# Performance work log

Measured on AMD Instinct MI355X. Metric: run time of the kernel, lower is better.

## Reference

```python
import jax, jax.numpy as jnp
import numpy as np

B, S, E, H = 2, 2048, 1024, 16
DH = E // H  # 64


def setup_inputs() -> dict:
    key = jax.random.key(0)
    ks = jax.random.split(key, 9)
    sc = 1.0 / np.sqrt(E)
    return {
        "x": jax.random.normal(ks[0], (B, S, E), dtype=jnp.float32),
        "Wq": jax.random.normal(ks[1], (E, E), dtype=jnp.float32) * sc,
        "bq": jax.random.normal(ks[2], (E,), dtype=jnp.float32) * 0.02,
        "Wk": jax.random.normal(ks[3], (E, E), dtype=jnp.float32) * sc,
        "bk": jax.random.normal(ks[4], (E,), dtype=jnp.float32) * 0.02,
        "Wv": jax.random.normal(ks[5], (E, E), dtype=jnp.float32) * sc,
        "bv": jax.random.normal(ks[6], (E,), dtype=jnp.float32) * 0.02,
        "Wo": jax.random.normal(ks[7], (E, E), dtype=jnp.float32) * sc,
        "bo": jax.random.normal(ks[8], (E,), dtype=jnp.float32) * 0.02,
    }


def reference(x, Wq, bq, Wk, bk, Wv, bv, Wo, bo):
    b, s, e = x.shape
    h, dh = H, e // H
    # NOTE: original torch code does .view(B, H, S, Dh) on the [B, S, E]
    # projection WITHOUT transposing first; we replicate that exact reshape.
    q = (x @ Wq.T + bq).reshape(b, h, s, dh)
    k = (x @ Wk.T + bk).reshape(b, h, s, dh)
    v = (x @ Wv.T + bv).reshape(b, h, s, dh)
    scale = 1.0 / jnp.sqrt(jnp.asarray(dh, dtype=x.dtype))
    scores = jax.nn.softmax(jnp.einsum("bhqd,bhkd->bhqk", q, k) * scale, axis=-1)
    out = jnp.einsum("bhqk,bhkd->bhqd", scores, v)  # [B,H,S,Dh]
    out = out.transpose(0, 2, 1, 3).reshape(b, s, e)  # matches torch transpose(1,2).view
    return out @ Wo.T + bo
```

## Files before the change

### kernel.cpp

```cpp
#include <hip/hip_runtime.h>
#include <hip/hip_bf16.h>
#include <stdint.h>

typedef __bf16 bf16x8 __attribute__((ext_vector_type(8)));
typedef float  f32x4  __attribute__((ext_vector_type(4)));
typedef float  f32x16 __attribute__((ext_vector_type(16)));
typedef __hip_bfloat16 bf16;

__device__ __forceinline__ void gll16(const void* g, void* l) {
    typedef const unsigned int __attribute__((address_space(1)))* gp_t;
    typedef unsigned int __attribute__((address_space(3)))* lp_t;
    __builtin_amdgcn_global_load_lds((gp_t)(g), (lp_t)(l), 16, 0, 0);
}

__device__ __forceinline__ float fexp2(float x) {
#if __has_builtin(__builtin_amdgcn_exp2f)
    return __builtin_amdgcn_exp2f(x);
#else
    float r; asm volatile("v_exp_f32 %0, %1" : "=v"(r) : "v"(x)); return r;
#endif
}

__device__ __forceinline__ float tsum16(const f32x16& v) {
    float a0 = v[0] + v[1],   a1 = v[2] + v[3];
    float a2 = v[4] + v[5],   a3 = v[6] + v[7];
    float a4 = v[8] + v[9],   a5 = v[10] + v[11];
    float a6 = v[12] + v[13], a7 = v[14] + v[15];
    float b0 = a0 + a1, b1 = a2 + a3, b2 = a4 + a5, b3 = a6 + a7;
    return (b0 + b1) + (b2 + b3);
}

__global__ __launch_bounds__(256) void prep_convert(
    const float* __restrict__ x,
    const float* __restrict__ wq, const float* __restrict__ wk,
    const float* __restrict__ wv, const float* __restrict__ wo,
    bf16* __restrict__ Xb, bf16* __restrict__ Wcat, bf16* __restrict__ Wob)
{
    int i = blockIdx.x * blockDim.x + threadIdx.x;
    int base = i * 4;
    const float* src; bf16* dst;
    if      (base < 4194304) { src = x  + base;             dst = Xb   + base; }
    else if (base < 5242880) { src = wq + (base - 4194304); dst = Wcat + (base - 4194304); }
    else if (base < 6291456) { src = wk + (base - 5242880); dst = Wcat + 1048576 + (base - 5242880); }
    else if (base < 7340032) { src = wv + (base - 6291456); dst = Wcat + 2097152 + (base - 6291456); }
    else                     { src = wo + (base - 7340032); dst = Wob  + (base - 7340032); }
    float4 v = *(const float4*)src;
    union { bf16 h[4]; ushort4 u; } cv;
    cv.h[0] = __float2bfloat16(v.x);
    cv.h[1] = __float2bfloat16(v.y);
    cv.h[2] = __float2bfloat16(v.z);
    cv.h[3] = __float2bfloat16(v.w);
    *(ushort4*)dst = cv.u;
}

__global__ __launch_bounds__(256, 2) void gemm_qkv(
    const bf16* __restrict__ X, const bf16* __restrict__ Wc,
    const float* __restrict__ bq, const float* __restrict__ bk, const float* __restrict__ bv,
    bf16* __restrict__ Pq, bf16* __restrict__ Pk, bf16* __restrict__ Pv)
{
    __shared__ __align__(16) bf16 Ab[2][128 * 32];
    __shared__ __align__(16) bf16 Bb[2][128 * 32];
    const int id = blockIdx.x;
    const int sid = (id & 7) * 96 + (id >> 3);
    const int t = threadIdx.x;
    const int lane = t & 63, w = t >> 6;
    const int lr = lane & 15, lg = lane >> 4;
    const int wr = w >> 1, wc = w & 1;
    const int row0 = (sid / 24) * 128, col0 = (sid % 24) * 128;

    f32x4 acc[4][4] = {};

    const char* Xc  = (const char*)X;
    const char* Wcc = (const char*)Wc;
    const int o0 = t * 16, o1 = o0 + 4096;
    const int ldsoff = w * 1024;

#define GSTAGE(K0, BUF)                                                               \
    {                                                                                 \
        char* AB = (char*)(Ab[BUF]);                                                  \
        char* BB = (char*)(Bb[BUF]);                                                  \
        gll16(Xc  + (size_t)(row0 + (o0 >> 6)) * 2048 + (size_t)(K0) * 2 + (o0 & 63), \
              AB + ldsoff);                                                           \
        gll16(Wcc + (size_t)(col0 + (o0 >> 6)) * 2048 + (size_t)(K0) * 2 + (o0 & 63), \
              BB + ldsoff);                                                           \
        gll16(Xc  + (size_t)(row0 + (o1 >> 6)) * 2048 + (size_t)(K0) * 2 + (o1 & 63), \
              AB + 4096 + ldsoff);                                                    \
        gll16(Wcc + (size_t)(col0 + (o1 >> 6)) * 2048 + (size_t)(K0) * 2 + (o1 & 63), \
              BB + 4096 + ldsoff);                                                    \
    }

    GSTAGE(0, 0);
    GSTAGE(32, 1);
    int cur = 0;
    for (int k0 = 0; k0 < 1024; k0 += 32) {
        if (k0 < 992) {
            asm volatile("s_waitcnt vmcnt(4)\n\ts_barrier" ::: "memory");
        } else {
            asm volatile("s_waitcnt vmcnt(0)\n\ts_barrier" ::: "memory");
        }
        const char* AbC = (const char*)(Ab[cur]);
        const char* BbC = (const char*)(Bb[cur]);
        bf16x8 af[4], bw[4];
        #pragma unroll
        for (int i = 0; i < 4; ++i)
            af[i] = *(const bf16x8*)(AbC + ((wr * 64 + i * 16 + lr) * 32 + lg * 8) * 2);
        #pragma unroll
        for (int j = 0; j < 4; ++j)
            bw[j] = *(const bf16x8*)(BbC + ((wc * 64 + j * 16 + lr) * 32 + lg * 8) * 2);
        #pragma unroll
        for (int i = 0; i < 4; ++i)
            #pragma unroll
            for (int j = 0; j < 4; ++j)
                acc[i][j] = __builtin_amdgcn_mfma_f32_16x16x32_bf16(af[i], bw[j], acc[i][j], 0, 0, 0);
        __builtin_amdgcn_s_barrier();
        if (k0 + 64 < 1024) GSTAGE(k0 + 64, cur);
        cur ^= 1;
    }
#undef GSTAGE

    const int mid = col0 >> 10;
    const float* bias = (mid == 0) ? bq : (mid == 1 ? bk : bv);
    bf16* Out = (mid == 0) ? Pq : (mid == 1 ? Pk : Pv);
    const float scale = (mid == 0) ? 0.125f * 1.44269504f : 1.0f;
    const int nc0 = col0 - (mid << 10) + wc * 64;
    const int mr0 = row0 + wr * 64;
    #pragma unroll
    for (int i = 0; i < 4; ++i)
        #pragma unroll
        for (int j = 0; j < 4; ++j) {
            int cc = nc0 + j * 16 + lr;
            float bsv = bias[cc];
            #pragma unroll
            for (int p = 0; p < 4; ++p) {
                int rr = mr0 + i * 16 + lg * 4 + p;
                Out[(size_t)rr * 1024 + cc] = __float2bfloat16((acc[i][j][p] + bsv) * scale);
            }
        }
}

__global__ __launch_bounds__(256) void transpose_v(const bf16* __restrict__ Pv, bf16* __restrict__ Vt)
{
    __shared__ bf16 tile[64][72];
    const int head = blockIdx.y;
    const int st   = blockIdx.x;
    const bf16* src = Pv + (size_t)head * 131072 + (size_t)st * 4096;
    bf16* dst = Vt + (size_t)head * 131072 + (size_t)st * 64;
    const int t = threadIdx.x;
    const int rr = t >> 2, c0 = (t & 3) * 16;
    #pragma unroll
    for (int u = 0; u < 2; ++u) {
        bf16x8 v = *(const bf16x8*)(src + rr * 64 + c0 + u * 8);
        #pragma unroll
        for (int e = 0; e < 8; ++e) tile[rr][c0 + u * 8 + e] = ((const bf16*)&v)[e];
    }
    __syncthreads();
    #pragma unroll
    for (int u = 0; u < 2; ++u) {
        bf16 ov[8];
        #pragma unroll
        for (int e = 0; e < 8; ++e) {
            int y = u * 8 + e;
            int z = (y & 3) | ((y & 8) >> 1) | ((y & 4) << 1);
            ov[e] = tile[c0 + z][rr];
        }
        *(bf16x8*)(dst + (size_t)rr * 2048 + c0 + u * 8) = *(const bf16x8*)ov;
    }
}

__global__ __launch_bounds__(512, 4) void attn_fwd(
    const bf16* __restrict__ Pq, const bf16* __restrict__ Pk,
    const bf16* __restrict__ Vt, bf16* __restrict__ Of)
{
    __shared__ __align__(16) bf16 Kl[2][128 * 64];
    __shared__ __align__(16) bf16 Vl[2][64 * 128];

    const int blk0 = blockIdx.x;
    const int blk = (blk0 & 7) * 64 + (blk0 >> 3);
    const int head = blk >> 4;
    const int qt = blk & 15;
    const int bb = head >> 4, hh = head & 15;
    const bf16* Qh = Pq + (size_t)head * 131072;
    const char* Khc = (const char*)(Pk + (size_t)head * 131072);
    const char* Vhc = (const char*)(Vt + (size_t)head * 131072);

    const int t = threadIdx.x;
    const int lane = t & 63, w = t >> 6;
    const int qg = w & 3, kh = w >> 2;
    const int ql = lane & 31, hi = lane >> 5;
    const int q0 = qt * 128 + qg * 32;

    bf16x8 qf[4];
    #pragma unroll
    for (int m = 0; m < 4; ++m)
        qf[m] = *(const bf16x8*)(Qh + (size_t)(q0 + ql) * 64 + m * 16 + hi * 8);

    f32x16 acc[2] = {};
    float l_run = 0.f;

    const int stg_key = t >> 3, stg_ks = t & 7;
    const int stg_d   = t >> 4, stg_vs = t & 15;
    const size_t kgo = (size_t)stg_key * 128 + ((stg_ks ^ (stg_key & 7)) * 16);
    const size_t vgo = (size_t)stg_d * 4096 + ((stg_vs ^ (stg_d & 15)) * 16);
    const int ldst = w * 1024;

#define STAGE(S0, BUF)                                                          \
    {                                                                           \
        char* KB = (char*)(Kl[BUF]);                                            \
        char* VB = (char*)(Vl[BUF]);                                            \
        _Pragma("unroll")                                                       \
        for (int qq = 0; qq < 2; ++qq) {                                        \
            gll16(Khc + (size_t)(S0) * 128 + (size_t)qq * 8192 + kgo,           \
                  KB + qq * 8192 + ldst);                                       \
            gll16(Vhc + (size_t)(S0) * 2 + (size_t)qq * 131072 + vgo,           \
                  VB + qq * 8192 + ldst);                                       \
        }                                                                       \
    }

    STAGE(0, 0);
    STAGE(128, 1);

    int cur = 0;
    for (int s0 = 0; s0 < 2048; s0 += 128) {
        if (s0 < 1920) {
            asm volatile("s_waitcnt vmcnt(4)\n\ts_barrier" ::: "memory");
        } else {
            asm volatile("s_waitcnt vmcnt(0)\n\ts_barrier" ::: "memory");
        }

        const char* KlC = (const char*)(Kl[cur]);
        const char* VlC = (const char*)(Vl[cur]);

        f32x16 sa[2] = {};
        __builtin_amdgcn_s_setprio(1);
        #pragma unroll
        for (int kb = 0; kb < 2; ++kb) {
            int row = kh * 64 + kb * 32 + ql;
            #pragma unroll
            for (int m = 0; m < 4; ++m) {
                int byt = row * 128 + ((32 * m + 16 * hi) ^ ((row & 7) << 4));
                bf16x8 kf = *(const bf16x8*)(KlC + byt);
                sa[kb] = __builtin_amdgcn_mfma_f32_32x32x16_bf16(kf, qf[m], sa[kb], 0, 0, 0);
            }
        }
        __builtin_amdgcn_s_setprio(0);

        #pragma unroll
        for (int kb = 0; kb < 2; ++kb)
            #pragma unroll
            for (int r = 0; r < 16; ++r)
                sa[kb][r] = fexp2(sa[kb][r]);
        l_run += tsum16(sa[0]) + tsum16(sa[1]);

        __builtin_amdgcn_s_setprio(1);
        #pragma unroll
        for (int sbl = 0; sbl < 4; ++sbl) {
            const int kb = sbl >> 1, par = (sbl & 1) * 8;
            const int sbg = kh * 4 + sbl;
            bf16x8 pa;
            #pragma unroll
            for (int e = 0; e < 8; ++e) pa[e] = (__bf16)sa[kb][par + e];
            #pragma unroll
            for (int db = 0; db < 2; ++db) {
                int row = db * 32 + ql;
                int byt = row * 256 + ((sbg * 32 + hi * 16) ^ ((row & 15) << 4));
                bf16x8 vf = *(const bf16x8*)(VlC + byt);
                acc[db] = __builtin_amdgcn_mfma_f32_32x32x16_bf16(vf, pa, acc[db], 0, 0, 0);
            }
        }
        __builtin_amdgcn_s_setprio(0);

        __builtin_amdgcn_s_barrier();
        if (s0 + 256 < 2048) STAGE(s0 + 256, cur);
        cur ^= 1;
    }
#undef STAGE

    l_run += __shfl_xor(l_run, 32);

    float* cb1 = (float*)Kl;
    float* cb2 = (float*)Vl;
    const int idx = qg * 64 + lane;
    if (kh == 1) {
        #pragma unroll
        for (int r = 0; r < 16; ++r) cb1[idx * 17 + r] = acc[0][r];
        cb1[idx * 17 + 16] = l_run;
        #pragma unroll
        for (int r = 0; r < 16; ++r) cb2[idx * 17 + r] = acc[1][r];
    }
    __syncthreads();
    if (kh == 0) {
        float inv = 1.0f / (l_run + cb1[idx * 17 + 16]);
        bf16* orow = Of + (size_t)(bb * 2048 + q0 + ql) * 1024 + hh * 64;
        #pragma unroll
        for (int db = 0; db < 2; ++db)
            #pragma unroll
            for (int g = 0; g < 4; ++g) {
                union { bf16 h[4]; ushort4 u; } ob;
                #pragma unroll
                for (int j = 0; j < 4; ++j) {
                    int r = 4 * g + j;
                    float p1 = (db == 0) ? cb1[idx * 17 + r] : cb2[idx * 17 + r];
                    ob.h[j] = __float2bfloat16((acc[db][r] + p1) * inv);
                }
                *(ushort4*)(orow + db * 32 + 8 * g + 4 * hi) = ob.u;
            }
    }
}

__global__ __launch_bounds__(256, 2) void gemm_out(
    const bf16* __restrict__ A, const bf16* __restrict__ W,
    const float* __restrict__ bo, float* __restrict__ C)
{
    __shared__ __align__(16) bf16 Ab[2][64 * 32];
    __shared__ __align__(16) bf16 Bb[2][128 * 32];
    const int id = blockIdx.x;
    const int sid = (id & 7) * 64 + (id >> 3);
    const int t = threadIdx.x;
    const int lane = t & 63, w = t >> 6;
    const int lr = lane & 15, lg = lane >> 4;
    const int wr = w >> 1, wc = w & 1;
    const int row0 = (sid >> 3) * 64, col0 = (sid & 7) * 128;

    f32x4 acc[2][4] = {};
    const char* Ac = (const char*)A;
    const char* Wc = (const char*)W;
    const int o0 = t * 16, o1 = o0 + 4096;
    const int ldsoff = w * 1024;

#define OSTAGE(K0, BUF)                                                               \
    {                                                                                 \
        char* AB = (char*)(Ab[BUF]);                                                  \
        char* BB = (char*)(Bb[BUF]);                                                  \
        gll16(Ac + (size_t)(row0 + (o0 >> 6)) * 2048 + (size_t)(K0) * 2 + (o0 & 63),  \
              AB + ldsoff);                                                           \
        gll16(Wc + (size_t)(col0 + (o0 >> 6)) * 2048 + (size_t)(K0) * 2 + (o0 & 63),  \
              BB + ldsoff);                                                           \
        gll16(Wc + (size_t)(col0 + (o1 >> 6)) * 2048 + (size_t)(K0) * 2 + (o1 & 63),  \
              BB + 4096 + ldsoff);                                                    \
    }

    OSTAGE(0, 0);
    OSTAGE(32, 1);
    int cur = 0;
    for (int k0 = 0; k0 < 1024; k0 += 32) {
        if (k0 < 992) {
            asm volatile("s_waitcnt vmcnt(3)\n\ts_barrier" ::: "memory");
        } else {
            asm volatile("s_waitcnt vmcnt(0)\n\ts_barrier" ::: "memory");
        }
        const char* AbC = (const char*)(Ab[cur]);
        const char* BbC = (const char*)(Bb[cur]);
        bf16x8 af[2], bw[4];
        #pragma unroll
        for (int i = 0; i < 2; ++i)
            af[i] = *(const bf16x8*)(AbC + ((wr * 32 + i * 16 + lr) * 32 + lg * 8) * 2);
        #pragma unroll
        for (int j = 0; j < 4; ++j)
            bw[j] = *(const bf16x8*)(BbC + ((wc * 64 + j * 16 + lr) * 32 + lg * 8) * 2);
        #pragma unroll
        for (int i = 0; i < 2; ++i)
            #pragma unroll
            for (int j = 0; j < 4; ++j)
                acc[i][j] = __builtin_amdgcn_mfma_f32_16x16x32_bf16(af[i], bw[j], acc[i][j], 0, 0, 0);
        __builtin_amdgcn_s_barrier();
        if (k0 + 64 < 1024) OSTAGE(k0 + 64, cur);
        cur ^= 1;
    }
#undef OSTAGE

    const int nc0 = col0 + wc * 64;
    const int mr0 = row0 + wr * 32;
    #pragma unroll
    for (int i = 0; i < 2; ++i)
        #pragma unroll
        for (int j = 0; j < 4; ++j) {
            int cc = nc0 + j * 16 + lr;
            float bsv = bo[cc];
            #pragma unroll
            for (int p = 0; p < 4; ++p) {
                int rr = mr0 + i * 16 + lg * 4 + p;
                C[(size_t)rr * 1024 + cc] = acc[i][j][p] + bsv;
            }
        }
}

extern "C" void kernel_launch(void* const* d_in, const int* in_sizes, int n_in,
                              void* d_out, int out_size, void* d_ws, size_t ws_size,
                              hipStream_t stream) {
    const float* x  = (const float*)d_in[0];
    const float* Wq = (const float*)d_in[1];
    const float* bq = (const float*)d_in[2];
    const float* Wk = (const float*)d_in[3];
    const float* bk = (const float*)d_in[4];
    const float* Wv = (const float*)d_in[5];
    const float* bv = (const float*)d_in[6];
    const float* Wo = (const float*)d_in[7];
    const float* bo = (const float*)d_in[8];
    float* out = (float*)d_out;

    char* ws = (char*)d_ws;
    bf16* Xb   = (bf16*)(ws + 0);
    bf16* Wcat = (bf16*)(ws + 8388608);
    bf16* Wob  = (bf16*)(ws + 14680064);
    bf16* Pq   = (bf16*)(ws + 16777216);
    bf16* Pk   = (bf16*)(ws + 25165824);
    bf16* Pv   = (bf16*)(ws + 33554432);
    bf16* Vt   = (bf16*)(ws + 0);
    bf16* Of   = (bf16*)(ws + 33554432);
    (void)ws_size; (void)in_sizes; (void)n_in; (void)out_size;

    prep_convert<<<8192, 256, 0, stream>>>(x, Wq, Wk, Wv, Wo, Xb, Wcat, Wob);
    gemm_qkv<<<768, 256, 0, stream>>>(Xb, Wcat, bq, bk, bv, Pq, Pk, Pv);
    transpose_v<<<dim3(32, 32), 256, 0, stream>>>(Pv, Vt);
    attn_fwd<<<512, 512, 0, stream>>>(Pq, Pk, Vt, Of);
    gemm_out<<<512, 256, 0, stream>>>(Of, Wob, bo, out);
}
```

Baseline: 111.3 us.

## Double QKV GEMM K-tile to 64 with XOR-swizzled LDS layout

The QKV projection GEMM now stages 64-wide K slices per buffer instead of 32, halving the number of barrier/wait iterations. Global loads are remapped so each row's 16-byte chunks are placed in LDS with an XOR swizzle on the row index, and the fragment reads apply the same swizzle to avoid LDS bank conflicts. LDS use doubles to 64 KB per block, which may limit the two-blocks-per-CU occupancy target.

```diff
diff --git a/kernel.cpp b/kernel.cpp
--- a/kernel.cpp
+++ b/kernel.cpp
@@ -58,8 +58,8 @@
     const float* __restrict__ bq, const float* __restrict__ bk, const float* __restrict__ bv,
     bf16* __restrict__ Pq, bf16* __restrict__ Pk, bf16* __restrict__ Pv)
 {
-    __shared__ __align__(16) bf16 Ab[2][128 * 32];
-    __shared__ __align__(16) bf16 Bb[2][128 * 32];
+    __shared__ __align__(16) bf16 Ab[2][128 * 64];
+    __shared__ __align__(16) bf16 Bb[2][128 * 64];
     const int id = blockIdx.x;
     const int sid = (id & 7) * 96 + (id >> 3);
     const int t = threadIdx.x;
@@ -72,48 +72,55 @@
 
     const char* Xc  = (const char*)X;
     const char* Wcc = (const char*)Wc;
-    const int o0 = t * 16, o1 = o0 + 4096;
-    const int ldsoff = w * 1024;
+    const int stg_r = t >> 3, stg_s = t & 7;
+    const size_t ago = (size_t)stg_r * 2048 + ((stg_s ^ (stg_r & 7)) * 16);
+    const int ldst = w * 1024;
 
 #define GSTAGE(K0, BUF)                                                               \
     {                                                                                 \
         char* AB = (char*)(Ab[BUF]);                                                  \
         char* BB = (char*)(Bb[BUF]);                                                  \
-        gll16(Xc  + (size_t)(row0 + (o0 >> 6)) * 2048 + (size_t)(K0) * 2 + (o0 & 63), \
-              AB + ldsoff);                                                           \
-        gll16(Wcc + (size_t)(col0 + (o0 >> 6)) * 2048 + (size_t)(K0) * 2 + (o0 & 63), \
-              BB + ldsoff);                                                           \
-        gll16(Xc  + (size_t)(row0 + (o1 >> 6)) * 2048 + (size_t)(K0) * 2 + (o1 & 63), \
-              AB + 4096 + ldsoff);                                                    \
-        gll16(Wcc + (size_t)(col0 + (o1 >> 6)) * 2048 + (size_t)(K0) * 2 + (o1 & 63), \
-              BB + 4096 + ldsoff);                                                    \
+        _Pragma("unroll")                                                             \
+        for (int qq = 0; qq < 4; ++qq) {                                              \
+            gll16(Xc  + (size_t)row0 * 2048 + (size_t)qq * 65536 + (size_t)(K0) * 2 + ago, \
+                  AB + qq * 4096 + ldst);                                             \
+            gll16(Wcc + (size_t)col0 * 2048 + (size_t)qq * 65536 + (size_t)(K0) * 2 + ago, \
+                  BB + qq * 4096 + ldst);                                             \
+        }                                                                             \
     }
 
     GSTAGE(0, 0);
-    GSTAGE(32, 1);
+    GSTAGE(64, 1);
     int cur = 0;
-    for (int k0 = 0; k0 < 1024; k0 += 32) {
-        if (k0 < 992) {
-            asm volatile("s_waitcnt vmcnt(4)\n\ts_barrier" ::: "memory");
+    for (int k0 = 0; k0 < 1024; k0 += 64) {
+        if (k0 < 960) {
+            asm volatile("s_waitcnt vmcnt(8)\n\ts_barrier" ::: "memory");
         } else {
             asm volatile("s_waitcnt vmcnt(0)\n\ts_barrier" ::: "memory");
         }
         const char* AbC = (const char*)(Ab[cur]);
         const char* BbC = (const char*)(Bb[cur]);
-        bf16x8 af[4], bw[4];
-        #pragma unroll
-        for (int i = 0; i < 4; ++i)
-            af[i] = *(const bf16x8*)(AbC + ((wr * 64 + i * 16 + lr) * 32 + lg * 8) * 2);
-        #pragma unroll
-        for (int j = 0; j < 4; ++j)
-            bw[j] = *(const bf16x8*)(BbC + ((wc * 64 + j * 16 + lr) * 32 + lg * 8) * 2);
-        #pragma unroll
-        for (int i = 0; i < 4; ++i)
-            #pragma unroll
-            for (int j = 0; j < 4; ++j)
-                acc[i][j] = __builtin_amdgcn_mfma_f32_16x16x32_bf16(af[i], bw[j], acc[i][j], 0, 0, 0);
+        #pragma unroll
+        for (int kk = 0; kk < 2; ++kk) {
+            bf16x8 af[4], bw[4];
+            #pragma unroll
+            for (int i = 0; i < 4; ++i) {
+                int row = wr * 64 + i * 16 + lr;
+                af[i] = *(const bf16x8*)(AbC + row * 128 + ((kk * 64 + lg * 16) ^ ((row & 7) << 4)));
+            }
+            #pragma unroll
+            for (int j = 0; j < 4; ++j) {
+                int row = wc * 64 + j * 16 + lr;
+                bw[j] = *(const bf16x8*)(BbC + row * 128 + ((kk * 64 + lg * 16) ^ ((row & 7) << 4)));
+            }
+            #pragma unroll
+            for (int i = 0; i < 4; ++i)
+                #pragma unroll
+                for (int j = 0; j < 4; ++j)
+                    acc[i][j] = __builtin_amdgcn_mfma_f32_16x16x32_bf16(af[i], bw[j], acc[i][j], 0, 0, 0);
+        }
         __builtin_amdgcn_s_barrier();
-        if (k0 + 64 < 1024) GSTAGE(k0 + 64, cur);
+        if (k0 + 128 < 1024) GSTAGE(k0 + 128, cur);
         cur ^= 1;
     }
 #undef GSTAGE
```

Measured after the change: 115.2 us. 3.6% more time.
